# Optimization experiments

Hardware: AMD Instinct MI355X
Metric: run time of the kernel (lower is better)

The kernel has to match this reference:

```python
import jax, jax.numpy as jnp
import numpy as np
from functools import partial

BETA = 0.5
THR = 1.0
NUM_STEPS = 25

@jax.custom_vjp
def spike_fn(x):
    # Heaviside spike; surrogate gradient (snntorch ATan, alpha=2) in bwd.
    return (x > 0).astype(x.dtype)

def _spike_fwd(x):
    return spike_fn(x), x

def _spike_bwd(x, g):
    return (g / (1.0 + (jnp.pi * x) ** 2),)

spike_fn.defvjp(_spike_fwd, _spike_bwd)

def setup_inputs() -> dict:
    key = jax.random.key(0)
    ks = jax.random.split(key, 12)
    B, I, H, O = 16384, 1024, 1024, 10
    s = 0.05
    return {
        "x":   jax.random.normal(ks[0], (B, I), jnp.float32),
        "W1":  jax.random.normal(ks[1], (H, I), jnp.float32) * s,
        "b1":  jax.random.normal(ks[2], (H,), jnp.float32) * s,
        "V1w": jax.random.normal(ks[3], (H, H), jnp.float32) * s,
        "V1b": jax.random.normal(ks[4], (H,), jnp.float32) * s,
        "W2":  jax.random.normal(ks[5], (H, H), jnp.float32) * s,
        "b2":  jax.random.normal(ks[6], (H,), jnp.float32) * s,
        "V2w": jax.random.normal(ks[7], (H, H), jnp.float32) * s,
        "V2b": jax.random.normal(ks[8], (H,), jnp.float32) * s,
        "W3":  jax.random.normal(ks[9], (O, H), jnp.float32) * s,
        "b3":  jax.random.normal(ks[10], (O,), jnp.float32) * s,
    }

def reference(x, W1, b1, V1w, V1b, W2, b2, V2w, V2b, W3, b3):
    B = x.shape[0]
    H = W1.shape[0]
    cur1 = x @ W1.T + b1  # loop-invariant: fc1(x) recomputed identically each step

    def step(carry, _):
        spk1, mem1, spk2, mem2, ssum = carry
        # RLeaky layer 1: soft reset based on previous mem, recurrent linear on prev spikes
        reset1 = (mem1 > THR).astype(mem1.dtype)
        mem1 = BETA * mem1 + cur1 + spk1 @ V1w.T + V1b - reset1 * THR
        spk1 = spike_fn(mem1 - THR)
        cur2 = spk1 @ W2.T + b2
        reset2 = (mem2 > THR).astype(mem2.dtype)
        mem2 = BETA * mem2 + cur2 + spk2 @ V2w.T + V2b - reset2 * THR
        spk2 = spike_fn(mem2 - THR)
        return (spk1, mem1, spk2, mem2, ssum + spk2), None

    z = jnp.zeros((B, H), x.dtype)
    init = (z, z, z, z, z)
    (s1, m1, s2, m2, spk_sum), _ = jax.lax.scan(step, init, None, length=NUM_STEPS)
    return (spk_sum / NUM_STEPS) @ W3.T + b3
```

## Files before the change

### kernel.cpp

```cpp
#include <hip/hip_runtime.h>


#pragma clang fp contract(off)

#define HDIM 1024
#define BATCH 16384
#define NSTEP 25
#define BMR 128
#define BNC 64
#define BK 16
#define KC 512

__device__ __forceinline__ void stage_a_f32(const float* __restrict__ g, float* s,
                                            int tid, int kt) {
  int row = tid & 127, c = tid >> 7;
  const float* src = g + (size_t)row * HDIM + kt * BK + c * 8;
  float4 v0 = *(const float4*)(src);
  float4 v1 = *(const float4*)(src + 4);
  int k0 = c * 8;
  s[(k0 + 0) * BMR + row] = v0.x; s[(k0 + 1) * BMR + row] = v0.y;
  s[(k0 + 2) * BMR + row] = v0.z; s[(k0 + 3) * BMR + row] = v0.w;
  s[(k0 + 4) * BMR + row] = v1.x; s[(k0 + 5) * BMR + row] = v1.y;
  s[(k0 + 6) * BMR + row] = v1.z; s[(k0 + 7) * BMR + row] = v1.w;
}

__device__ __forceinline__ void stage_a_u8(const unsigned char* __restrict__ g, float* s,
                                           int tid, int kt) {
  int row = tid & 127, c = tid >> 7;
  unsigned long long v =
      *(const unsigned long long*)(g + (size_t)row * HDIM + kt * BK + c * 8);
  int k0 = c * 8;
#pragma unroll
  for (int q = 0; q < 8; ++q)
    s[(k0 + q) * BMR + row] = (float)((v >> (8 * q)) & 0xFFull);
}

__device__ __forceinline__ void stage_b(const float* __restrict__ g, float* s,
                                        int tid, int kt) {
  int row = tid & 63, c = tid >> 6;
  float4 v = *(const float4*)(g + (size_t)row * HDIM + kt * BK + c * 4);
  int k0 = c * 4;
  s[(k0 + 0) * BNC + row] = v.x; s[(k0 + 1) * BNC + row] = v.y;
  s[(k0 + 2) * BNC + row] = v.z; s[(k0 + 3) * BNC + row] = v.w;
}

template <bool AU8>
__device__ __forceinline__ void kpass(const void* __restrict__ Ag,
                                      const float* __restrict__ Bg,
                                      float* sA, float* sB, int tid, int m0, int n0,
                                      float csum[4][8]) {
  float p[4][8];
#pragma unroll
  for (int m = 0; m < 4; ++m)
#pragma unroll
    for (int n = 0; n < 8; ++n) { csum[m][n] = 0.0f; p[m][n] = 0.0f; }

#pragma unroll 1
  for (int kt = 0; kt < HDIM / BK; ++kt) {
    if (AU8) stage_a_u8((const unsigned char*)Ag, sA, tid, kt);
    else     stage_a_f32((const float*)Ag, sA, tid, kt);
    stage_b(Bg, sB, tid, kt);
    __syncthreads();
#pragma unroll
    for (int k = 0; k < BK; ++k) {
      float a[4], b[8];
      *(float4*)&a[0] = *(const float4*)&sA[k * BMR + m0];
      *(float4*)&b[0] = *(const float4*)&sB[k * BNC + n0];
      *(float4*)&b[4] = *(const float4*)&sB[k * BNC + n0 + 4];
#pragma unroll
      for (int m = 0; m < 4; ++m)
#pragma unroll
        for (int n = 0; n < 8; ++n)
          p[m][n] = __builtin_fmaf(a[m], b[n], p[m][n]);
    }
    if (((kt + 1) * BK) % KC == 0) {
#pragma unroll
      for (int m = 0; m < 4; ++m)
#pragma unroll
        for (int n = 0; n < 8; ++n) { csum[m][n] = csum[m][n] + p[m][n]; p[m][n] = 0.0f; }
    }
    __syncthreads();
  }
}

__global__ __launch_bounds__(256) void gemm_cur(const float* __restrict__ A,
                                                const float* __restrict__ B,
                                                const float* __restrict__ bias,
                                                float* __restrict__ outv) {
  __shared__ float sA[BK * BMR];
  __shared__ float sB[BK * BNC];
  const int tid = threadIdx.x;
  const int m0 = (tid >> 3) * 4, n0 = (tid & 7) * 8;
  const int bm = blockIdx.y, bn = blockIdx.x;
  float csum[4][8];
  kpass<false>(A + (size_t)bm * BMR * HDIM, B + (size_t)bn * BNC * HDIM,
               sA, sB, tid, m0, n0, csum);
  const int colb = bn * BNC + n0;
  float4 bia0 = *(const float4*)&bias[colb];
  float4 bia1 = *(const float4*)&bias[colb + 4];
  const float bi[8] = {bia0.x, bia0.y, bia0.z, bia0.w, bia1.x, bia1.y, bia1.z, bia1.w};
#pragma unroll
  for (int m = 0; m < 4; ++m) {
    size_t idx = (size_t)(bm * BMR + m0 + m) * HDIM + colb;
    float o[8];
#pragma unroll
    for (int n = 0; n < 8; ++n) o[n] = csum[m][n] + bi[n];
    *(float4*)&outv[idx] = *(float4*)&o[0];
    *(float4*)&outv[idx + 4] = *(float4*)&o[4];
  }
}

__global__ __launch_bounds__(256) void gemm_l1(
    const unsigned char* __restrict__ A, const float* __restrict__ B,
    const float* __restrict__ vb, const float* __restrict__ cur1,
    float* __restrict__ memv, unsigned char* __restrict__ spk_out) {
  __shared__ float sA[BK * BMR];
  __shared__ float sB[BK * BNC];
  const int tid = threadIdx.x;
  const int m0 = (tid >> 3) * 4, n0 = (tid & 7) * 8;
  const int bm = blockIdx.y, bn = blockIdx.x;
  float csum[4][8];
  kpass<true>(A + (size_t)bm * BMR * HDIM, B + (size_t)bn * BNC * HDIM,
              sA, sB, tid, m0, n0, csum);
  const int colb = bn * BNC + n0;
  float4 v0 = *(const float4*)&vb[colb];
  float4 v1 = *(const float4*)&vb[colb + 4];
  const float vbv[8] = {v0.x, v0.y, v0.z, v0.w, v1.x, v1.y, v1.z, v1.w};
#pragma unroll
  for (int m = 0; m < 4; ++m) {
    size_t row = (size_t)(bm * BMR + m0 + m);
    size_t idx = row * HDIM + colb;
    float mo[8], au[8], tn[8];
    *(float4*)&mo[0] = *(const float4*)&memv[idx];
    *(float4*)&mo[4] = *(const float4*)&memv[idx + 4];
    *(float4*)&au[0] = *(const float4*)&cur1[idx];
    *(float4*)&au[4] = *(const float4*)&cur1[idx + 4];
    unsigned long long sv = 0;
#pragma unroll
    for (int n = 0; n < 8; ++n) {
      float reset = (mo[n] > 1.0f) ? 1.0f : 0.0f;
      float t = 0.5f * mo[n];
      t = t + au[n];
      t = t + csum[m][n];
      t = t + vbv[n];
      t = t - reset;
      tn[n] = t;
      sv |= ((unsigned long long)(((t - 1.0f) > 0.0f) ? 1 : 0)) << (8 * n);
    }
    *(float4*)&memv[idx] = *(float4*)&tn[0];
    *(float4*)&memv[idx + 4] = *(float4*)&tn[4];
    *(unsigned long long*)&spk_out[idx] = sv;
  }
}

__global__ __launch_bounds__(256) void gemm_l2f(
    const unsigned char* __restrict__ A1, const float* __restrict__ B1,
    const unsigned char* __restrict__ A2, const float* __restrict__ B2,
    const float* __restrict__ bias, const float* __restrict__ vb,
    float* __restrict__ memv, unsigned char* __restrict__ spk_out,
    unsigned char* __restrict__ ssum) {
  __shared__ float sA[BK * BMR];
  __shared__ float sB[BK * BNC];
  const int tid = threadIdx.x;
  const int m0 = (tid >> 3) * 4, n0 = (tid & 7) * 8;
  const int bm = blockIdx.y, bn = blockIdx.x;
  float dot1[4][8], csum[4][8];
  kpass<true>(A1 + (size_t)bm * BMR * HDIM, B1 + (size_t)bn * BNC * HDIM,
              sA, sB, tid, m0, n0, csum);
#pragma unroll
  for (int m = 0; m < 4; ++m)
#pragma unroll
    for (int n = 0; n < 8; ++n) dot1[m][n] = csum[m][n];
  __syncthreads();
  kpass<true>(A2 + (size_t)bm * BMR * HDIM, B2 + (size_t)bn * BNC * HDIM,
              sA, sB, tid, m0, n0, csum);
  const int colb = bn * BNC + n0;
  float4 b0 = *(const float4*)&bias[colb];
  float4 b1v = *(const float4*)&bias[colb + 4];
  const float bi[8] = {b0.x, b0.y, b0.z, b0.w, b1v.x, b1v.y, b1v.z, b1v.w};
  float4 v0 = *(const float4*)&vb[colb];
  float4 v1 = *(const float4*)&vb[colb + 4];
  const float vbv[8] = {v0.x, v0.y, v0.z, v0.w, v1.x, v1.y, v1.z, v1.w};
#pragma unroll
  for (int m = 0; m < 4; ++m) {
    size_t row = (size_t)(bm * BMR + m0 + m);
    size_t idx = row * HDIM + colb;
    float mo[8], tn[8];
    *(float4*)&mo[0] = *(const float4*)&memv[idx];
    *(float4*)&mo[4] = *(const float4*)&memv[idx + 4];
    unsigned long long sv = 0;
#pragma unroll
    for (int n = 0; n < 8; ++n) {
      float reset = (mo[n] > 1.0f) ? 1.0f : 0.0f;
      float cur2 = dot1[m][n] + bi[n];
      float t = 0.5f * mo[n];
      t = t + cur2;
      t = t + csum[m][n];
      t = t + vbv[n];
      t = t - reset;
      tn[n] = t;
      sv |= ((unsigned long long)(((t - 1.0f) > 0.0f) ? 1 : 0)) << (8 * n);
    }
    *(float4*)&memv[idx] = *(float4*)&tn[0];
    *(float4*)&memv[idx + 4] = *(float4*)&tn[4];
    *(unsigned long long*)&spk_out[idx] = sv;
    unsigned long long old = *(unsigned long long*)&ssum[idx];
    unsigned long long ns = 0;
#pragma unroll
    for (int n = 0; n < 8; ++n) {
      unsigned char c = (unsigned char)(((old >> (8 * n)) & 0xFF) + ((sv >> (8 * n)) & 1));
      ns |= ((unsigned long long)c) << (8 * n);
    }
    *(unsigned long long*)&ssum[idx] = ns;
  }
}

__global__ __launch_bounds__(256) void out_blas(const unsigned char* __restrict__ ssum,
                                                const float* __restrict__ W3,
                                                const float* __restrict__ b3,
                                                float* __restrict__ out) {
  int t = blockIdx.x * 256 + threadIdx.x;
  int b = t >> 4, o = t & 15;
  if (o >= 10) return;
  const unsigned char* sp = ssum + (size_t)b * HDIM;
  const float* wp = W3 + (size_t)o * HDIM;
  float csum = 0.0f, p = 0.0f;
#pragma unroll 4
  for (int k = 0; k < HDIM; ++k) {
    float sv = (float)sp[k] / 25.0f;
    p = __builtin_fmaf(sv, wp[k], p);
    if ((k + 1) % KC == 0) { csum = csum + p; p = 0.0f; }
  }
  out[(size_t)b * 10 + o] = csum + b3[o];
}

extern "C" void kernel_launch(void* const* d_in, const int* in_sizes, int n_in,
                              void* d_out, int out_size, void* d_ws, size_t ws_size,
                              hipStream_t stream) {
  const float* x = (const float*)d_in[0];
  const float* W1 = (const float*)d_in[1];
  const float* b1 = (const float*)d_in[2];
  const float* V1w = (const float*)d_in[3];
  const float* V1b = (const float*)d_in[4];
  const float* W2 = (const float*)d_in[5];
  const float* b2 = (const float*)d_in[6];
  const float* V2w = (const float*)d_in[7];
  const float* V2b = (const float*)d_in[8];
  const float* W3 = (const float*)d_in[9];
  const float* b3 = (const float*)d_in[10];
  float* out = (float*)d_out;

  char* ws = (char*)d_ws;
  const size_t per_row = (size_t)HDIM * 4 * 3 + (size_t)HDIM * 5;
  size_t rows = BATCH;
  while (rows > 128 && rows * per_row > ws_size) rows >>= 1;
  const int nchunk = (int)(BATCH / rows);
  const size_t RH = rows * (size_t)HDIM;

  size_t off = 0;
  float* cur1 = (float*)(ws + off); off += RH * 4;
  float* mem1 = (float*)(ws + off); off += RH * 4;
  float* mem2 = (float*)(ws + off); off += RH * 4;
  unsigned char *spk1[2], *spk2[2];
  spk1[0] = (unsigned char*)(ws + off); off += RH;
  spk1[1] = (unsigned char*)(ws + off); off += RH;
  spk2[0] = (unsigned char*)(ws + off); off += RH;
  spk2[1] = (unsigned char*)(ws + off); off += RH;
  unsigned char* ssum = (unsigned char*)(ws + off); off += RH;

  dim3 grid(HDIM / BNC, (unsigned)(rows / BMR));

  for (int c = 0; c < nchunk; ++c) {
    const float* xc = x + (size_t)c * RH;
    float* outc = out + (size_t)c * rows * 10;

    hipMemsetAsync(mem1, 0, RH * 4, stream);
    hipMemsetAsync(mem2, 0, RH * 4, stream);
    hipMemsetAsync(ssum, 0, RH, stream);
    hipMemsetAsync(spk1[0], 0, RH, stream);
    hipMemsetAsync(spk2[0], 0, RH, stream);

    gemm_cur<<<grid, 256, 0, stream>>>(xc, W1, b1, cur1);

    for (int t = 0; t < NSTEP; ++t) {
      int rd = t & 1, wr = rd ^ 1;
      gemm_l1<<<grid, 256, 0, stream>>>(spk1[rd], V1w, V1b, cur1, mem1, spk1[wr]);
      gemm_l2f<<<grid, 256, 0, stream>>>(spk1[wr], W2, spk2[rd], V2w, b2, V2b,
                                         mem2, spk2[wr], ssum);
    }
    out_blas<<<(unsigned)(rows * 16 / 256), 256, 0, stream>>>(ssum, W3, b3, outc);
  }
}
```

Baseline: 34.16 ms.

## Double-buffer shared-memory tiles with register prefetch and skip zero-spike step-0 GEMMs

Raises the K tile to 32 and double-buffers the shared-memory A/B tiles, prefetching the next tile into registers while the current one is computed, so only one barrier is needed per K tile. At step 0 the layer-1 recurrent GEMM is replaced by a purely elementwise kernel, and the layer-2 recurrent GEMM is skipped, because the previous spikes are known to be zero. This removes several memsets and about two full GEMM passes per chunk. The cost is higher register and LDS use, which may lower occupancy.

```diff
diff --git a/kernel.cpp b/kernel.cpp
--- a/kernel.cpp
+++ b/kernel.cpp
@@ -8,65 +8,89 @@
 #define NSTEP 25
 #define BMR 128
 #define BNC 64
-#define BK 16
+#define BK 32
+#define NKT (HDIM / BK)
 #define KC 512
 
-__device__ __forceinline__ void stage_a_f32(const float* __restrict__ g, float* s,
-                                            int tid, int kt) {
+__device__ __forceinline__ void load_a_f32(const float* __restrict__ g, int tid,
+                                           int kt, float r[16]) {
   int row = tid & 127, c = tid >> 7;
+  const float* src = g + (size_t)row * HDIM + kt * BK + c * 16;
+  *(float4*)&r[0] = *(const float4*)(src);
+  *(float4*)&r[4] = *(const float4*)(src + 4);
+  *(float4*)&r[8] = *(const float4*)(src + 8);
+  *(float4*)&r[12] = *(const float4*)(src + 12);
+}
+
+__device__ __forceinline__ void load_a_u8(const unsigned char* __restrict__ g, int tid,
+                                          int kt, float r[16]) {
+  int row = tid & 127, c = tid >> 7;
+  const unsigned char* src = g + (size_t)row * HDIM + kt * BK + c * 16;
+  unsigned long long v0 = *(const unsigned long long*)(src);
+  unsigned long long v1 = *(const unsigned long long*)(src + 8);
+#pragma unroll
+  for (int q = 0; q < 8; ++q) {
+    r[q] = (float)((v0 >> (8 * q)) & 0xFFull);
+    r[8 + q] = (float)((v1 >> (8 * q)) & 0xFFull);
+  }
+}
+
+__device__ __forceinline__ void load_b(const float* __restrict__ g, int tid,
+                                       int kt, float r[8]) {
+  int row = tid & 63, c = tid >> 6;
   const float* src = g + (size_t)row * HDIM + kt * BK + c * 8;
-  float4 v0 = *(const float4*)(src);
-  float4 v1 = *(const float4*)(src + 4);
-  int k0 = c * 8;
-  s[(k0 + 0) * BMR + row] = v0.x; s[(k0 + 1) * BMR + row] = v0.y;
-  s[(k0 + 2) * BMR + row] = v0.z; s[(k0 + 3) * BMR + row] = v0.w;
-  s[(k0 + 4) * BMR + row] = v1.x; s[(k0 + 5) * BMR + row] = v1.y;
-  s[(k0 + 6) * BMR + row] = v1.z; s[(k0 + 7) * BMR + row] = v1.w;
-}
-
-__device__ __forceinline__ void stage_a_u8(const unsigned char* __restrict__ g, float* s,
-                                           int tid, int kt) {
-  int row = tid & 127, c = tid >> 7;
-  unsigned long long v =
-      *(const unsigned long long*)(g + (size_t)row * HDIM + kt * BK + c * 8);
-  int k0 = c * 8;
-#pragma unroll
-  for (int q = 0; q < 8; ++q)
-    s[(k0 + q) * BMR + row] = (float)((v >> (8 * q)) & 0xFFull);
-}
-
-__device__ __forceinline__ void stage_b(const float* __restrict__ g, float* s,
-                                        int tid, int kt) {
-  int row = tid & 63, c = tid >> 6;
-  float4 v = *(const float4*)(g + (size_t)row * HDIM + kt * BK + c * 4);
-  int k0 = c * 4;
-  s[(k0 + 0) * BNC + row] = v.x; s[(k0 + 1) * BNC + row] = v.y;
-  s[(k0 + 2) * BNC + row] = v.z; s[(k0 + 3) * BNC + row] = v.w;
+  *(float4*)&r[0] = *(const float4*)(src);
+  *(float4*)&r[4] = *(const float4*)(src + 4);
+}
+
+__device__ __forceinline__ void write_a(float* sA, int tid, const float r[16]) {
+  int row = tid & 127, k0 = (tid >> 7) * 16;
+#pragma unroll
+  for (int q = 0; q < 16; ++q) sA[(k0 + q) * BMR + row] = r[q];
+}
+
+__device__ __forceinline__ void write_b(float* sB, int tid, const float r[8]) {
+  int row = tid & 63, k0 = (tid >> 6) * 8;
+#pragma unroll
+  for (int q = 0; q < 8; ++q) sB[(k0 + q) * BNC + row] = r[q];
 }
 
 template <bool AU8>
 __device__ __forceinline__ void kpass(const void* __restrict__ Ag,
                                       const float* __restrict__ Bg,
-                                      float* sA, float* sB, int tid, int m0, int n0,
-                                      float csum[4][8]) {
+                                      float* sA0, float* sB0, float* sA1, float* sB1,
+                                      int tid, int m0, int n0, float csum[4][8]) {
   float p[4][8];
 #pragma unroll
   for (int m = 0; m < 4; ++m)
 #pragma unroll
     for (int n = 0; n < 8; ++n) { csum[m][n] = 0.0f; p[m][n] = 0.0f; }
 
+  float ra[16], rb[8];
+  if (AU8) load_a_u8((const unsigned char*)Ag, tid, 0, ra);
+  else     load_a_f32((const float*)Ag, tid, 0, ra);
+  load_b(Bg, tid, 0, rb);
+  write_a(sA0, tid, ra);
+  write_b(sB0, tid, rb);
+  __syncthreads();
+
 #pragma unroll 1
-  for (int kt = 0; kt < HDIM / BK; ++kt) {
-    if (AU8) stage_a_u8((const unsigned char*)Ag, sA, tid, kt);
-    else     stage_a_f32((const float*)Ag, sA, tid, kt);
-    stage_b(Bg, sB, tid, kt);
-    __syncthreads();
+  for (int kt = 0; kt < NKT; ++kt) {
+    float* cA = (kt & 1) ? sA1 : sA0;
+    float* cB = (kt & 1) ? sB1 : sB0;
+    float* nA = (kt & 1) ? sA0 : sA1;
+    float* nB = (kt & 1) ? sB0 : sB1;
+    if (kt + 1 < NKT) {
+      if (AU8) load_a_u8((const unsigned char*)Ag, tid, kt + 1, ra);
+      else     load_a_f32((const float*)Ag, tid, kt + 1, ra);
+      load_b(Bg, tid, kt + 1, rb);
+    }
 #pragma unroll
     for (int k = 0; k < BK; ++k) {
       float a[4], b[8];
-      *(float4*)&a[0] = *(const float4*)&sA[k * BMR + m0];
-      *(float4*)&b[0] = *(const float4*)&sB[k * BNC + n0];
-      *(float4*)&b[4] = *(const float4*)&sB[k * BNC + n0 + 4];
+      *(float4*)&a[0] = *(const float4*)&cA[k * BMR + m0];
+      *(float4*)&b[0] = *(const float4*)&cB[k * BNC + n0];
+      *(float4*)&b[4] = *(const float4*)&cB[k * BNC + n0 + 4];
 #pragma unroll
       for (int m = 0; m < 4; ++m)
 #pragma unroll
@@ -78,6 +102,10 @@
       for (int m = 0; m < 4; ++m)
 #pragma unroll
         for (int n = 0; n < 8; ++n) { csum[m][n] = csum[m][n] + p[m][n]; p[m][n] = 0.0f; }
+    }
+    if (kt + 1 < NKT) {
+      write_a(nA, tid, ra);
+      write_b(nB, tid, rb);
     }
     __syncthreads();
   }
@@ -87,14 +115,13 @@
                                                 const float* __restrict__ B,
                                                 const float* __restrict__ bias,
                                                 float* __restrict__ outv) {
-  __shared__ float sA[BK * BMR];
-  __shared__ float sB[BK * BNC];
+  __shared__ float sA0[BK * BMR], sB0[BK * BNC], sA1[BK * BMR], sB1[BK * BNC];
   const int tid = threadIdx.x;
   const int m0 = (tid >> 3) * 4, n0 = (tid & 7) * 8;
   const int bm = blockIdx.y, bn = blockIdx.x;
   float csum[4][8];
   kpass<false>(A + (size_t)bm * BMR * HDIM, B + (size_t)bn * BNC * HDIM,
-               sA, sB, tid, m0, n0, csum);
+               sA0, sB0, sA1, sB1, tid, m0, n0, csum);
   const int colb = bn * BNC + n0;
   float4 bia0 = *(const float4*)&bias[colb];
   float4 bia1 = *(const float4*)&bias[colb + 4];
@@ -110,26 +137,52 @@
   }
 }
 
+__global__ __launch_bounds__(256) void l1_t0(const float* __restrict__ cur1,
+                                             const float* __restrict__ vb,
+                                             float* __restrict__ memv,
+                                             unsigned char* __restrict__ spk_out) {
+  size_t i = ((size_t)blockIdx.x * 256 + threadIdx.x) * 8;
+  int col = (int)(i & (HDIM - 1));
+  float au[8], tn[8];
+  *(float4*)&au[0] = *(const float4*)&cur1[i];
+  *(float4*)&au[4] = *(const float4*)&cur1[i + 4];
+  float4 v0 = *(const float4*)&vb[col];
+  float4 v1 = *(const float4*)&vb[col + 4];
+  const float vbv[8] = {v0.x, v0.y, v0.z, v0.w, v1.x, v1.y, v1.z, v1.w};
+  unsigned long long sv = 0;
+#pragma unroll
+  for (int n = 0; n < 8; ++n) {
+    float t = 0.5f * 0.0f;
+    t = t + au[n];
+    t = t + 0.0f;
+    t = t + vbv[n];
+    t = t - 0.0f;
+    tn[n] = t;
+    sv |= ((unsigned long long)(((t - 1.0f) > 0.0f) ? 1 : 0)) << (8 * n);
+  }
+  *(float4*)&memv[i] = *(float4*)&tn[0];
+  *(float4*)&memv[i + 4] = *(float4*)&tn[4];
+  *(unsigned long long*)&spk_out[i] = sv;
+}
+
 __global__ __launch_bounds__(256) void gemm_l1(
     const unsigned char* __restrict__ A, const float* __restrict__ B,
     const float* __restrict__ vb, const float* __restrict__ cur1,
     float* __restrict__ memv, unsigned char* __restrict__ spk_out) {
-  __shared__ float sA[BK * BMR];
-  __shared__ float sB[BK * BNC];
+  __shared__ float sA0[BK * BMR], sB0[BK * BNC], sA1[BK * BMR], sB1[BK * BNC];
   const int tid = threadIdx.x;
   const int m0 = (tid >> 3) * 4, n0 = (tid & 7) * 8;
   const int bm = blockIdx.y, bn = blockIdx.x;
   float csum[4][8];
   kpass<true>(A + (size_t)bm * BMR * HDIM, B + (size_t)bn * BNC * HDIM,
-              sA, sB, tid, m0, n0, csum);
+              sA0, sB0, sA1, sB1, tid, m0, n0, csum);
   const int colb = bn * BNC + n0;
   float4 v0 = *(const float4*)&vb[colb];
   float4 v1 = *(const float4*)&vb[colb + 4];
   const float vbv[8] = {v0.x, v0.y, v0.z, v0.w, v1.x, v1.y, v1.z, v1.w};
 #pragma unroll
   for (int m = 0; m < 4; ++m) {
-    size_t row = (size_t)(bm * BMR + m0 + m);
-    size_t idx = row * HDIM + colb;
+    size_t idx = (size_t)(bm * BMR + m0 + m) * HDIM + colb;
     float mo[8], au[8], tn[8];
     *(float4*)&mo[0] = *(const float4*)&memv[idx];
     *(float4*)&mo[4] = *(const float4*)&memv[idx + 4];
@@ -158,22 +211,23 @@
     const unsigned char* __restrict__ A2, const float* __restrict__ B2,
     const float* __restrict__ bias, const float* __restrict__ vb,
     float* __restrict__ memv, unsigned char* __restrict__ spk_out,
-    unsigned char* __restrict__ ssum) {
-  __shared__ float sA[BK * BMR];
-  __shared__ float sB[BK * BNC];
+    unsigned char* __restrict__ ssum, int skip2) {
+  __shared__ float sA0[BK * BMR], sB0[BK * BNC], sA1[BK * BMR], sB1[BK * BNC];
   const int tid = threadIdx.x;
   const int m0 = (tid >> 3) * 4, n0 = (tid & 7) * 8;
   const int bm = blockIdx.y, bn = blockIdx.x;
   float dot1[4][8], csum[4][8];
   kpass<true>(A1 + (size_t)bm * BMR * HDIM, B1 + (size_t)bn * BNC * HDIM,
-              sA, sB, tid, m0, n0, csum);
-#pragma unroll
-  for (int m = 0; m < 4; ++m)
-#pragma unroll
-    for (int n = 0; n < 8; ++n) dot1[m][n] = csum[m][n];
-  __syncthreads();
-  kpass<true>(A2 + (size_t)bm * BMR * HDIM, B2 + (size_t)bn * BNC * HDIM,
-              sA, sB, tid, m0, n0, csum);
+              sA0, sB0, sA1, sB1, tid, m0, n0, dot1);
+  if (skip2) {
+#pragma unroll
+    for (int m = 0; m < 4; ++m)
+#pragma unroll
+      for (int n = 0; n < 8; ++n) csum[m][n] = 0.0f;
+  } else {
+    kpass<true>(A2 + (size_t)bm * BMR * HDIM, B2 + (size_t)bn * BNC * HDIM,
+                sA0, sB0, sA1, sB1, tid, m0, n0, csum);
+  }
   const int colb = bn * BNC + n0;
   float4 b0 = *(const float4*)&bias[colb];
   float4 b1v = *(const float4*)&bias[colb + 4];
@@ -183,8 +237,7 @@
   const float vbv[8] = {v0.x, v0.y, v0.z, v0.w, v1.x, v1.y, v1.z, v1.w};
 #pragma unroll
   for (int m = 0; m < 4; ++m) {
-    size_t row = (size_t)(bm * BMR + m0 + m);
-    size_t idx = row * HDIM + colb;
+    size_t idx = (size_t)(bm * BMR + m0 + m) * HDIM + colb;
     float mo[8], tn[8];
     *(float4*)&mo[0] = *(const float4*)&memv[idx];
     *(float4*)&mo[4] = *(const float4*)&memv[idx + 4];
@@ -274,19 +327,20 @@
     const float* xc = x + (size_t)c * RH;
     float* outc = out + (size_t)c * rows * 10;
 
-    hipMemsetAsync(mem1, 0, RH * 4, stream);
     hipMemsetAsync(mem2, 0, RH * 4, stream);
     hipMemsetAsync(ssum, 0, RH, stream);
-    hipMemsetAsync(spk1[0], 0, RH, stream);
-    hipMemsetAsync(spk2[0], 0, RH, stream);
 
     gemm_cur<<<grid, 256, 0, stream>>>(xc, W1, b1, cur1);
 
     for (int t = 0; t < NSTEP; ++t) {
       int rd = t & 1, wr = rd ^ 1;
-      gemm_l1<<<grid, 256, 0, stream>>>(spk1[rd], V1w, V1b, cur1, mem1, spk1[wr]);
+      if (t == 0) {
+        l1_t0<<<(unsigned)(RH / (256 * 8)), 256, 0, stream>>>(cur1, V1b, mem1, spk1[wr]);
+      } else {
+        gemm_l1<<<grid, 256, 0, stream>>>(spk1[rd], V1w, V1b, cur1, mem1, spk1[wr]);
+      }
       gemm_l2f<<<grid, 256, 0, stream>>>(spk1[wr], W2, spk2[rd], V2w, b2, V2b,
-                                         mem2, spk2[wr], ssum);
+                                         mem2, spk2[wr], ssum, t == 0 ? 1 : 0);
     }
     out_blas<<<(unsigned)(rows * 16 / 256), 256, 0, stream>>>(ssum, W3, b3, outc);
   }
```

Result: slower. 40.12 ms (+17.4%).

## Skip zero-spike recurrent GEMMs at first step and double K tile

Applied to the files above, without the earlier changes.

At timestep zero the previous spikes and membranes are all zero, so the layer-1 recurrent GEMM is replaced by a pure elementwise kernel and the layer-2 recurrent GEMM is skipped. This also removes several memsets. Separately, the K tile grows from 16 to 32, which halves the number of sync/stage iterations at the cost of more shared memory per block. The fp32 add order is kept so the spike thresholds stay bitwise identical.

```diff
diff --git a/kernel.cpp b/kernel.cpp
--- a/kernel.cpp
+++ b/kernel.cpp
@@ -8,40 +8,54 @@
 #define NSTEP 25
 #define BMR 128
 #define BNC 64
-#define BK 16
+#define BK 32
+#define NKT (HDIM / BK)
 #define KC 512
 
 __device__ __forceinline__ void stage_a_f32(const float* __restrict__ g, float* s,
                                             int tid, int kt) {
   int row = tid & 127, c = tid >> 7;
+  const float* src = g + (size_t)row * HDIM + kt * BK + c * 16;
+  float4 v0 = *(const float4*)(src);
+  float4 v1 = *(const float4*)(src + 4);
+  float4 v2 = *(const float4*)(src + 8);
+  float4 v3 = *(const float4*)(src + 12);
+  int k0 = c * 16;
+  s[(k0 + 0) * BMR + row] = v0.x;  s[(k0 + 1) * BMR + row] = v0.y;
+  s[(k0 + 2) * BMR + row] = v0.z;  s[(k0 + 3) * BMR + row] = v0.w;
+  s[(k0 + 4) * BMR + row] = v1.x;  s[(k0 + 5) * BMR + row] = v1.y;
+  s[(k0 + 6) * BMR + row] = v1.z;  s[(k0 + 7) * BMR + row] = v1.w;
+  s[(k0 + 8) * BMR + row] = v2.x;  s[(k0 + 9) * BMR + row] = v2.y;
+  s[(k0 + 10) * BMR + row] = v2.z; s[(k0 + 11) * BMR + row] = v2.w;
+  s[(k0 + 12) * BMR + row] = v3.x; s[(k0 + 13) * BMR + row] = v3.y;
+  s[(k0 + 14) * BMR + row] = v3.z; s[(k0 + 15) * BMR + row] = v3.w;
+}
+
+__device__ __forceinline__ void stage_a_u8(const unsigned char* __restrict__ g, float* s,
+                                           int tid, int kt) {
+  int row = tid & 127, c = tid >> 7;
+  const unsigned char* src = g + (size_t)row * HDIM + kt * BK + c * 16;
+  unsigned long long v0 = *(const unsigned long long*)(src);
+  unsigned long long v1 = *(const unsigned long long*)(src + 8);
+  int k0 = c * 16;
+#pragma unroll
+  for (int q = 0; q < 8; ++q) {
+    s[(k0 + q) * BMR + row] = (float)((v0 >> (8 * q)) & 0xFFull);
+    s[(k0 + 8 + q) * BMR + row] = (float)((v1 >> (8 * q)) & 0xFFull);
+  }
+}
+
+__device__ __forceinline__ void stage_b(const float* __restrict__ g, float* s,
+                                        int tid, int kt) {
+  int row = tid & 63, c = tid >> 6;
   const float* src = g + (size_t)row * HDIM + kt * BK + c * 8;
   float4 v0 = *(const float4*)(src);
   float4 v1 = *(const float4*)(src + 4);
   int k0 = c * 8;
-  s[(k0 + 0) * BMR + row] = v0.x; s[(k0 + 1) * BMR + row] = v0.y;
-  s[(k0 + 2) * BMR + row] = v0.z; s[(k0 + 3) * BMR + row] = v0.w;
-  s[(k0 + 4) * BMR + row] = v1.x; s[(k0 + 5) * BMR + row] = v1.y;
-  s[(k0 + 6) * BMR + row] = v1.z; s[(k0 + 7) * BMR + row] = v1.w;
-}
-
-__device__ __forceinline__ void stage_a_u8(const unsigned char* __restrict__ g, float* s,
-                                           int tid, int kt) {
-  int row = tid & 127, c = tid >> 7;
-  unsigned long long v =
-      *(const unsigned long long*)(g + (size_t)row * HDIM + kt * BK + c * 8);
-  int k0 = c * 8;
-#pragma unroll
-  for (int q = 0; q < 8; ++q)
-    s[(k0 + q) * BMR + row] = (float)((v >> (8 * q)) & 0xFFull);
-}
-
-__device__ __forceinline__ void stage_b(const float* __restrict__ g, float* s,
-                                        int tid, int kt) {
-  int row = tid & 63, c = tid >> 6;
-  float4 v = *(const float4*)(g + (size_t)row * HDIM + kt * BK + c * 4);
-  int k0 = c * 4;
-  s[(k0 + 0) * BNC + row] = v.x; s[(k0 + 1) * BNC + row] = v.y;
-  s[(k0 + 2) * BNC + row] = v.z; s[(k0 + 3) * BNC + row] = v.w;
+  s[(k0 + 0) * BNC + row] = v0.x; s[(k0 + 1) * BNC + row] = v0.y;
+  s[(k0 + 2) * BNC + row] = v0.z; s[(k0 + 3) * BNC + row] = v0.w;
+  s[(k0 + 4) * BNC + row] = v1.x; s[(k0 + 5) * BNC + row] = v1.y;
+  s[(k0 + 6) * BNC + row] = v1.z; s[(k0 + 7) * BNC + row] = v1.w;
 }
 
 template <bool AU8>
@@ -56,7 +70,7 @@
     for (int n = 0; n < 8; ++n) { csum[m][n] = 0.0f; p[m][n] = 0.0f; }
 
 #pragma unroll 1
-  for (int kt = 0; kt < HDIM / BK; ++kt) {
+  for (int kt = 0; kt < NKT; ++kt) {
     if (AU8) stage_a_u8((const unsigned char*)Ag, sA, tid, kt);
     else     stage_a_f32((const float*)Ag, sA, tid, kt);
     stage_b(Bg, sB, tid, kt);
@@ -110,6 +124,34 @@
   }
 }
 
+__global__ __launch_bounds__(256) void l1_t0(const float* __restrict__ cur1,
+                                             const float* __restrict__ vb,
+                                             float* __restrict__ memv,
+                                             unsigned char* __restrict__ spk_out) {
+  size_t i = ((size_t)blockIdx.x * 256 + threadIdx.x) * 8;
+  int col = (int)(i & (HDIM - 1));
+  float au[8], tn[8];
+  *(float4*)&au[0] = *(const float4*)&cur1[i];
+  *(float4*)&au[4] = *(const float4*)&cur1[i + 4];
+  float4 v0 = *(const float4*)&vb[col];
+  float4 v1 = *(const float4*)&vb[col + 4];
+  const float vbv[8] = {v0.x, v0.y, v0.z, v0.w, v1.x, v1.y, v1.z, v1.w};
+  unsigned long long sv = 0;
+#pragma unroll
+  for (int n = 0; n < 8; ++n) {
+    float t = 0.5f * 0.0f;
+    t = t + au[n];
+    t = t + 0.0f;
+    t = t + vbv[n];
+    t = t - 0.0f;
+    tn[n] = t;
+    sv |= ((unsigned long long)(((t - 1.0f) > 0.0f) ? 1 : 0)) << (8 * n);
+  }
+  *(float4*)&memv[i] = *(float4*)&tn[0];
+  *(float4*)&memv[i + 4] = *(float4*)&tn[4];
+  *(unsigned long long*)&spk_out[i] = sv;
+}
+
 __global__ __launch_bounds__(256) void gemm_l1(
     const unsigned char* __restrict__ A, const float* __restrict__ B,
     const float* __restrict__ vb, const float* __restrict__ cur1,
@@ -128,8 +170,7 @@
   const float vbv[8] = {v0.x, v0.y, v0.z, v0.w, v1.x, v1.y, v1.z, v1.w};
 #pragma unroll
   for (int m = 0; m < 4; ++m) {
-    size_t row = (size_t)(bm * BMR + m0 + m);
-    size_t idx = row * HDIM + colb;
+    size_t idx = (size_t)(bm * BMR + m0 + m) * HDIM + colb;
     float mo[8], au[8], tn[8];
     *(float4*)&mo[0] = *(const float4*)&memv[idx];
     *(float4*)&mo[4] = *(const float4*)&memv[idx + 4];
@@ -158,7 +199,7 @@
     const unsigned char* __restrict__ A2, const float* __restrict__ B2,
     const float* __restrict__ bias, const float* __restrict__ vb,
     float* __restrict__ memv, unsigned char* __restrict__ spk_out,
-    unsigned char* __restrict__ ssum) {
+    unsigned char* __restrict__ ssum, int skip2) {
   __shared__ float sA[BK * BMR];
   __shared__ float sB[BK * BNC];
   const int tid = threadIdx.x;
@@ -166,14 +207,17 @@
   const int bm = blockIdx.y, bn = blockIdx.x;
   float dot1[4][8], csum[4][8];
   kpass<true>(A1 + (size_t)bm * BMR * HDIM, B1 + (size_t)bn * BNC * HDIM,
-              sA, sB, tid, m0, n0, csum);
-#pragma unroll
-  for (int m = 0; m < 4; ++m)
-#pragma unroll
-    for (int n = 0; n < 8; ++n) dot1[m][n] = csum[m][n];
-  __syncthreads();
-  kpass<true>(A2 + (size_t)bm * BMR * HDIM, B2 + (size_t)bn * BNC * HDIM,
-              sA, sB, tid, m0, n0, csum);
+              sA, sB, tid, m0, n0, dot1);
+  if (skip2) {
+#pragma unroll
+    for (int m = 0; m < 4; ++m)
+#pragma unroll
+      for (int n = 0; n < 8; ++n) csum[m][n] = 0.0f;
+  } else {
+    __syncthreads();
+    kpass<true>(A2 + (size_t)bm * BMR * HDIM, B2 + (size_t)bn * BNC * HDIM,
+                sA, sB, tid, m0, n0, csum);
+  }
   const int colb = bn * BNC + n0;
   float4 b0 = *(const float4*)&bias[colb];
   float4 b1v = *(const float4*)&bias[colb + 4];
@@ -183,8 +227,7 @@
   const float vbv[8] = {v0.x, v0.y, v0.z, v0.w, v1.x, v1.y, v1.z, v1.w};
 #pragma unroll
   for (int m = 0; m < 4; ++m) {
-    size_t row = (size_t)(bm * BMR + m0 + m);
-    size_t idx = row * HDIM + colb;
+    size_t idx = (size_t)(bm * BMR + m0 + m) * HDIM + colb;
     float mo[8], tn[8];
     *(float4*)&mo[0] = *(const float4*)&memv[idx];
     *(float4*)&mo[4] = *(const float4*)&memv[idx + 4];
@@ -274,19 +317,20 @@
     const float* xc = x + (size_t)c * RH;
     float* outc = out + (size_t)c * rows * 10;
 
-    hipMemsetAsync(mem1, 0, RH * 4, stream);
     hipMemsetAsync(mem2, 0, RH * 4, stream);
     hipMemsetAsync(ssum, 0, RH, stream);
-    hipMemsetAsync(spk1[0], 0, RH, stream);
-    hipMemsetAsync(spk2[0], 0, RH, stream);
 
     gemm_cur<<<grid, 256, 0, stream>>>(xc, W1, b1, cur1);
 
     for (int t = 0; t < NSTEP; ++t) {
       int rd = t & 1, wr = rd ^ 1;
-      gemm_l1<<<grid, 256, 0, stream>>>(spk1[rd], V1w, V1b, cur1, mem1, spk1[wr]);
+      if (t == 0) {
+        l1_t0<<<(unsigned)(RH / (256 * 8)), 256, 0, stream>>>(cur1, V1b, mem1, spk1[wr]);
+      } else {
+        gemm_l1<<<grid, 256, 0, stream>>>(spk1[rd], V1w, V1b, cur1, mem1, spk1[wr]);
+      }
       gemm_l2f<<<grid, 256, 0, stream>>>(spk1[wr], W2, spk2[rd], V2w, b2, V2b,
-                                         mem2, spk2[wr], ssum);
+                                         mem2, spk2[wr], ssum, t == 0 ? 1 : 0);
     }
     out_blas<<<(unsigned)(rows * 16 / 256), 256, 0, stream>>>(ssum, W3, b3, outc);
   }
```

Result: faster. 30.75 ms (-10.0%).
